# Optimization experiments

Hardware: AMD Instinct MI355X
Metric: run time of the kernel (lower is better)

The kernel has to match this reference:

```python
import jax, jax.numpy as jnp
import numpy as np

FRACTION = 0.33  # from attn_type='query_selector_0.33'


def setup_inputs() -> dict:
    key = jax.random.key(0)
    k1, k2, k3, k4 = jax.random.split(key, 4)
    B, L, DIM_VAL, DIM_ATTN = 8, 4096, 64, 64
    scale = 1.0 / np.sqrt(DIM_VAL).astype(np.float32)
    x = jax.random.normal(k1, (B, L, DIM_VAL), dtype=jnp.float32)
    Wq = jax.random.normal(k2, (DIM_VAL, DIM_ATTN), dtype=jnp.float32) * scale
    Wk = jax.random.normal(k3, (DIM_VAL, DIM_ATTN), dtype=jnp.float32) * scale
    Wv = jax.random.normal(k4, (DIM_VAL, DIM_VAL), dtype=jnp.float32) * scale
    return {"x": x, "Wq": Wq, "Wk": Wk, "Wv": Wv}


def reference(x, Wq, Wk, Wv):
    # Projections (bias-free Linears)
    Q = jnp.einsum('bld,de->ble', x, Wq)  # [B, L, Da]
    K = jnp.einsum('bld,de->ble', x, Wk)  # [B, L, Da]
    V = jnp.einsum('bld,de->ble', x, Wv)  # [B, L, Dv]

    B, L_Q, Da = Q.shape
    l_Q = int((1.0 - FRACTION) * L_Q)  # static: shapes known at trace time

    # keys.topk(l_Q, dim=1).values -> per-channel top-l_Q along seq; mean over them
    K_top = jax.lax.top_k(jnp.swapaxes(K, 1, 2), l_Q)[0]  # [B, Da, l_Q]
    K_reduce = K_top.mean(axis=-1)                         # [B, Da]

    # score each query against the reduced key; pick top-l_Q queries
    sqk = jnp.einsum('bd,bld->bl', K_reduce, Q)            # [B, L_Q]
    indices = jax.lax.top_k(sqk, l_Q)[1]                   # [B, l_Q] int32

    # gather sampled queries
    Q_sample = jnp.take_along_axis(Q, indices[:, :, None], axis=1)  # [B, l_Q, Da]

    # dense attention for the sampled queries only
    scores = jnp.einsum('bqd,bkd->bqk', Q_sample, K) / jnp.sqrt(jnp.asarray(Da, Q.dtype))
    attn = jax.nn.softmax(scores, axis=-1)                 # [B, l_Q, L]
    out_sel = jnp.einsum('bqk,bkv->bqv', attn, V)          # [B, l_Q, Dv]

    # mean-filled result, scatter attention outputs to selected rows
    mean_values = V.mean(axis=-2)                          # [B, Dv]
    result = jnp.broadcast_to(mean_values[:, None, :], (B, L_Q, V.shape[-1]))
    result = result.at[jnp.arange(B)[:, None], indices].set(out_sel)
    return result
```

## Files before the change

kernel.cpp:

```cpp
#include <hip/hip_runtime.h>
#include <hip/hip_bf16.h>
#include <math.h>

#define BATCH 8
#define SEQ   4096
#define DIM   64
#define LQ    2744
#define QPB   128
#define NQB   22
#define QPAD  2816
#define KS    4
#define L2E   1.4426950408889634f
#define QSC   0.1803368801111204f

typedef _Float16 half8 __attribute__((ext_vector_type(8)));
typedef short    bs8   __attribute__((ext_vector_type(8)));
typedef float    fx16  __attribute__((ext_vector_type(16)));
typedef unsigned short ushort_t;

union UH { uint4 u4; half8 h; };
union UB { unsigned u[4]; uint4 u4; bs8 s; };

__device__ __forceinline__ unsigned pack_bf16(float a, float b) {
    __hip_bfloat162 h = __float22bfloat162_rn(make_float2(a, b));
    union { __hip_bfloat162 h; unsigned u; } cv; cv.h = h; return cv.u;
}

__device__ __forceinline__ unsigned f2sort(float f) {
    unsigned u = __float_as_uint(f);
    return (u & 0x80000000u) ? ~u : (u | 0x80000000u);
}
__device__ __forceinline__ float sort2f(unsigned u) {
    return __uint_as_float((u & 0x80000000u) ? (u & 0x7FFFFFFFu) : ~u);
}

__device__ void radix_select_4096(const unsigned* u, int k, unsigned* hist,
                                  unsigned* scan, unsigned* res) {
    const int t = threadIdx.x;
    if (t == 0) { res[0] = 0u; res[1] = (unsigned)k; }
    for (int pass = 3; pass >= 0; --pass) {
        const int shift = pass * 8;
        hist[t] = 0u;
        __syncthreads();
        const unsigned pref  = res[0];
        const unsigned kk    = res[1];
        const unsigned hmask = (pass == 3) ? 0u : (0xFFFFFFFFu << (shift + 8));
        for (int i = t; i < 4096; i += 256) {
            unsigned ui = u[i];
            if ((ui & hmask) == pref) atomicAdd(&hist[(ui >> shift) & 255u], 1u);
        }
        __syncthreads();
        const unsigned h = hist[t];
        unsigned s = h;
        scan[t] = s;
        __syncthreads();
#pragma unroll
        for (int ofs = 1; ofs < 256; ofs <<= 1) {
            unsigned add = (t + ofs < 256) ? scan[t + ofs] : 0u;
            __syncthreads();
            s += add;
            scan[t] = s;
            __syncthreads();
        }
        if (s >= kk && (s - h) < kk) {
            res[0] = pref | ((unsigned)t << shift);
            res[1] = kk - (s - h);
        }
        __syncthreads();
    }
}

__global__ __launch_bounds__(256) void proj_kernel(
    const float* __restrict__ x,  const float* __restrict__ Wq,
    const float* __restrict__ Wk, const float* __restrict__ Wv,
    float* __restrict__ Q, float* __restrict__ Kt,
    _Float16* __restrict__ Qh, _Float16* __restrict__ Kh,
    ushort_t* __restrict__ Vt, float* __restrict__ meanacc) {
    const int rt = blockIdx.x, b = blockIdx.y, t = threadIdx.x;
    __shared__ float4 xs4[64 * 17];
    __shared__ float  red[4][64];
    {
        const float4* xg = (const float4*)(x + ((size_t)b * SEQ + rt * 64) * DIM);
        for (int i = 0; i < 4; ++i) {
            int s = t + 256 * i;
            xs4[(s >> 4) * 17 + (s & 15)] = xg[s];
        }
    }
    __syncthreads();
    const int ch = t & 63, rg = t >> 6;
    float accq[16], acck[16], accv[16];
#pragma unroll
    for (int i = 0; i < 16; ++i) { accq[i] = 0.f; acck[i] = 0.f; accv[i] = 0.f; }
    for (int dc = 0; dc < 4; ++dc) {
        float wq[16], wk[16], wv[16];
#pragma unroll
        for (int dd = 0; dd < 16; ++dd) {
            int d = dc * 16 + dd;
            wq[dd] = Wq[d * 64 + ch]; wk[dd] = Wk[d * 64 + ch]; wv[dd] = Wv[d * 64 + ch];
        }
        for (int r = 0; r < 16; ++r) {
            const int row = rg * 16 + r;
            const float4* xr = &xs4[row * 17 + dc * 4];
            float xv[16];
            float4 a0 = xr[0], a1 = xr[1], a2 = xr[2], a3 = xr[3];
            xv[0]=a0.x; xv[1]=a0.y; xv[2]=a0.z; xv[3]=a0.w;
            xv[4]=a1.x; xv[5]=a1.y; xv[6]=a1.z; xv[7]=a1.w;
            xv[8]=a2.x; xv[9]=a2.y; xv[10]=a2.z; xv[11]=a2.w;
            xv[12]=a3.x; xv[13]=a3.y; xv[14]=a3.z; xv[15]=a3.w;
#pragma unroll
            for (int dd = 0; dd < 16; ++dd) {
                accq[r] = fmaf(xv[dd], wq[dd], accq[r]);
                acck[r] = fmaf(xv[dd], wk[dd], acck[r]);
                accv[r] = fmaf(xv[dd], wv[dd], accv[r]);
            }
        }
    }
    const int rowbase = rt * 64 + rg * 16;
    float sv = 0.f;
#pragma unroll
    for (int r = 0; r < 16; ++r) {
        size_t o = ((size_t)b * SEQ + rowbase + r) * DIM + ch;
        Q[o]  = accq[r];
        Qh[o] = (_Float16)(accq[r] * QSC);
        Kh[o] = (_Float16)acck[r];
        sv += accv[r];
    }
    float4* ktp = (float4*)(Kt + ((size_t)b * 64 + ch) * SEQ + rowbase);
    ktp[0] = make_float4(acck[0], acck[1], acck[2], acck[3]);
    ktp[1] = make_float4(acck[4], acck[5], acck[6], acck[7]);
    ktp[2] = make_float4(acck[8], acck[9], acck[10], acck[11]);
    ktp[3] = make_float4(acck[12], acck[13], acck[14], acck[15]);
    {
        unsigned pk[8];
#pragma unroll
        for (int i = 0; i < 8; ++i) pk[i] = pack_bf16(accv[2*i], accv[2*i+1]);
        uint4* vp = (uint4*)(Vt + ((size_t)(b * 64 + ch)) * SEQ + rowbase);
        vp[0] = make_uint4(pk[0], pk[1], pk[4], pk[5]);
        vp[1] = make_uint4(pk[2], pk[3], pk[6], pk[7]);
    }
    red[rg][ch] = sv;
    __syncthreads();
    if (rg == 0)
        atomicAdd(&meanacc[b * 64 + ch],
                  red[0][ch] + red[1][ch] + red[2][ch] + red[3][ch]);
}

__global__ __launch_bounds__(256) void kmean_kernel(const float* __restrict__ Kt,
                                                    float* __restrict__ Kred) {
    __shared__ unsigned u[4096];
    __shared__ unsigned hist[256];
    __shared__ unsigned scan[256];
    __shared__ unsigned res[2];
    __shared__ float rsum[4];
    const int bc = blockIdx.x, t = threadIdx.x;
    const float4* c4 = (const float4*)(Kt + (size_t)bc * SEQ);
    for (int i = t; i < 1024; i += 256) {
        float4 v = c4[i];
        u[i*4+0] = f2sort(v.x); u[i*4+1] = f2sort(v.y);
        u[i*4+2] = f2sort(v.z); u[i*4+3] = f2sort(v.w);
    }
    __syncthreads();
    radix_select_4096(u, LQ, hist, scan, res);
    const unsigned Tu = res[0];
    const int krem = (int)res[1];
    float loc = 0.f;
    for (int i = t; i < 4096; i += 256)
        if (u[i] > Tu) loc += sort2f(u[i]);
    for (int msk = 1; msk < 64; msk <<= 1) loc += __shfl_xor(loc, msk, 64);
    if ((t & 63) == 0) rsum[t >> 6] = loc;
    __syncthreads();
    if (t == 0) {
        float s = rsum[0] + rsum[1] + rsum[2] + rsum[3] + (float)krem * sort2f(Tu);
        Kred[bc] = s / (float)LQ;
    }
}

__global__ __launch_bounds__(256) void sqk_kernel(const float* __restrict__ Q,
                                                  const float* __restrict__ Kred,
                                                  float* __restrict__ sqk) {
    const int b = blockIdx.y, l = blockIdx.x * 256 + threadIdx.x;
    __shared__ float kr[64];
    if (threadIdx.x < 64) kr[threadIdx.x] = Kred[b * 64 + threadIdx.x];
    __syncthreads();
    const float4* q = (const float4*)(Q + ((size_t)b * SEQ + l) * DIM);
    float s = 0.f;
#pragma unroll
    for (int i = 0; i < 16; ++i) {
        float4 v = q[i];
        s = fmaf(v.x, kr[i*4+0], s); s = fmaf(v.y, kr[i*4+1], s);
        s = fmaf(v.z, kr[i*4+2], s); s = fmaf(v.w, kr[i*4+3], s);
    }
    sqk[b * SEQ + l] = s;
}

__global__ __launch_bounds__(256) void select_kernel(const float* __restrict__ sqk,
                                                     int* __restrict__ sel) {
    __shared__ unsigned u[4096];
    __shared__ unsigned hist[256];
    __shared__ unsigned scan[256];
    __shared__ unsigned res[2];
    __shared__ int eq_idx[256];
    __shared__ int cnts[2];
    const int b = blockIdx.x, t = threadIdx.x;
    const float* col = sqk + (size_t)b * SEQ;
    for (int i = t; i < 4096; i += 256) u[i] = f2sort(col[i]);
    if (t < 2) cnts[t] = 0;
    __syncthreads();
    radix_select_4096(u, LQ, hist, scan, res);
    const unsigned Tu = res[0];
    const int krem = (int)res[1];
    int* selb = sel + b * QPAD;
    for (int i = t; i < 4096; i += 256) {
        unsigned ui = u[i];
        if (ui > Tu) {
            int p = atomicAdd(&cnts[0], 1);
            selb[p] = i;
        } else if (ui == Tu) {
            int p = atomicAdd(&cnts[1], 1);
            if (p < 256) eq_idx[p] = i;
        }
    }
    __syncthreads();
    if (t == 0) {
        int ng = cnts[0];
        int ne = cnts[1] < 256 ? cnts[1] : 256;
        for (int i = 1; i < ne; ++i) {
            int v = eq_idx[i], j = i - 1;
            while (j >= 0 && eq_idx[j] > v) { eq_idx[j+1] = eq_idx[j]; --j; }
            eq_idx[j+1] = v;
        }
        for (int j = 0; j < krem; ++j) selb[ng + j] = eq_idx[j];
        for (int j = LQ; j < QPAD; ++j) selb[j] = selb[LQ - 1];
    }
}

__global__ __launch_bounds__(256) void fill_kernel(const float* __restrict__ meanacc,
                                                   float* __restrict__ out) {
    const int idx = blockIdx.x * 256 + threadIdx.x;
    if (idx >= BATCH * SEQ * 16) return;
    const int b = idx >> 16, c = idx & 15;
    const float inv = 1.0f / (float)SEQ;
    float4 mv = make_float4(meanacc[b*64 + c*4 + 0] * inv,
                            meanacc[b*64 + c*4 + 1] * inv,
                            meanacc[b*64 + c*4 + 2] * inv,
                            meanacc[b*64 + c*4 + 3] * inv);
    ((float4*)out)[idx] = mv;
}

__global__ __launch_bounds__(256) void attn_kernel(
    const ushort_t* __restrict__ Qh, const ushort_t* __restrict__ Kh,
    const ushort_t* __restrict__ Vt, const int* __restrict__ sel,
    float* __restrict__ pl, float* __restrict__ pout) {
    const int qt = blockIdx.x, ks = blockIdx.y, b = blockIdx.z;
    const int t = threadIdx.x, w = t >> 6, lane = t & 63;
    const int col = lane & 31, h = lane >> 5;

    __shared__ ushort_t Ktile[2][32 * 64];
    __shared__ ushort_t Vtile[2][32 * 64];

    half8 qf[4];
    {
        const int q = qt * QPB + w * 32 + col;
        const int row = sel[b * QPAD + q];
        const uint4* qg = (const uint4*)(Qh + ((size_t)b * SEQ + row) * DIM);
#pragma unroll
        for (int m = 0; m < 4; ++m) { UH u; u.u4 = qg[2 * m + h]; qf[m] = u.h; }
    }

    fx16 O0, O1;
#pragma unroll
    for (int r = 0; r < 16; ++r) { O0[r] = 0.f; O1[r] = 0.f; }
    float l = 0.f;

    const int srow = t >> 3, sgr = t & 7;
    const int lg = sgr ^ (srow & 7);
    const int vD = lg >> 2, vc = (lg >> 1) & 1, vh = lg & 1;
    const size_t kgbase = ((size_t)b * SEQ + ks * 1024 + srow) * DIM + 8 * lg;
    const size_t vgbase = ((size_t)(b * DIM + srow + 32 * vD)) * SEQ
                          + ks * 1024 + vc * 16 + vh * 8;

    uint4 kreg = *(const uint4*)(Kh + kgbase);
    uint4 vreg = *(const uint4*)(Vt + vgbase);

    for (int tile = 0; tile < 32; ++tile) {
        const int buf = tile & 1;
        *(uint4*)&Ktile[buf][srow * 64 + sgr * 8] = kreg;
        *(uint4*)&Vtile[buf][srow * 64 + sgr * 8] = vreg;
        __syncthreads();
        if (tile < 31) {
            kreg = *(const uint4*)(Kh + kgbase + (size_t)(tile + 1) * 32 * DIM);
            vreg = *(const uint4*)(Vt + vgbase + (size_t)(tile + 1) * 32);
        }
        fx16 S;
#pragma unroll
        for (int r = 0; r < 16; ++r) S[r] = 0.f;
#pragma unroll
        for (int m = 0; m < 4; ++m) {
            UH kf;
            kf.u4 = *(const uint4*)&Ktile[buf][col * 64 + 8 * ((2 * m + h) ^ (col & 7))];
            S = __builtin_amdgcn_mfma_f32_32x32x16_f16(kf.h, qf[m], S, 0, 0, 0);
        }
        float p[16];
#pragma unroll
        for (int r = 0; r < 16; ++r) p[r] = exp2f(S[r]);
#pragma unroll
        for (int r = 0; r < 16; ++r) l += p[r];
        UB A0, A1;
#pragma unroll
        for (int v = 0; v < 4; ++v) {
            A0.u[v] = pack_bf16(p[2 * v],     p[2 * v + 1]);
            A1.u[v] = pack_bf16(p[8 + 2 * v], p[8 + 2 * v + 1]);
        }
#pragma unroll
        for (int D = 0; D < 2; ++D) {
            fx16& O = D ? O1 : O0;
#pragma unroll
            for (int c = 0; c < 2; ++c) {
                UB vf;
                vf.u4 = *(const uint4*)&Vtile[buf][col * 64 + 8 * ((4 * D + 2 * c + h) ^ (col & 7))];
                O = __builtin_amdgcn_mfma_f32_32x32x16_bf16(c ? A1.s : A0.s, vf.s, O, 0, 0, 0);
            }
        }
    }

    l += __shfl_xor(l, 32);

    const int qg0 = qt * QPB + w * 32;
    const size_t base = (size_t)b * QPAD + qg0;
#pragma unroll
    for (int D = 0; D < 2; ++D) {
        const fx16& O = D ? O1 : O0;
#pragma unroll
        for (int r = 0; r < 16; ++r) {
            const int q = (r & 3) + 8 * (r >> 2) + 4 * h;
            atomicAdd(&pout[(base + q) * DIM + D * 32 + col], O[r]);
        }
    }
    if (h == 0) atomicAdd(&pl[base + col], l);
}

__global__ __launch_bounds__(256) void comb_kernel(
    const float* __restrict__ pl, const float* __restrict__ pout,
    const int* __restrict__ sel, float* __restrict__ out) {
    const int idx = blockIdx.x * 256 + threadIdx.x;
    if (idx >= BATCH * LQ * 16) return;
    const int b = idx / (LQ * 16);
    const int r = idx % (LQ * 16);
    const int qs = r >> 4, c = r & 15;
    const size_t s0 = (size_t)b * QPAD + qs;
    const float inv = 1.0f / pl[s0];
    float4 a = ((const float4*)(pout + s0 * DIM))[c];
    float4 o = make_float4(a.x * inv, a.y * inv, a.z * inv, a.w * inv);
    const int row = sel[b * QPAD + qs];
    ((float4*)(out + ((size_t)b * SEQ + row) * DIM))[c] = o;
}

extern "C" void kernel_launch(void* const* d_in, const int* in_sizes, int n_in,
                              void* d_out, int out_size, void* d_ws, size_t ws_size,
                              hipStream_t stream) {
    const float* x  = (const float*)d_in[0];
    const float* Wq = (const float*)d_in[1];
    const float* Wk = (const float*)d_in[2];
    const float* Wv = (const float*)d_in[3];
    float* out = (float*)d_out;
    char* wsb  = (char*)d_ws;

    float*    Q       = (float*)(wsb);
    _Float16* Qh      = (_Float16*)(wsb + 8388608);
    _Float16* Kh      = (_Float16*)(wsb + 12582912);
    ushort_t* Vt      = (ushort_t*)(wsb + 16777216);
    float*    meanacc = (float*)(wsb + 20971520);
    float*    Kred    = (float*)(wsb + 20973568);
    float*    sqk     = (float*)(wsb + 20975616);
    int*      sel     = (int*)(wsb + 21106688);
    float*    Kt      = (float*)(wsb + 21196800);
    float*    pout    = (float*)(wsb + 21196800);
    float*    pl      = (float*)(wsb + 21196800 + 5767168);

    hipMemsetAsync(meanacc, 0, 512 * sizeof(float), stream);
    proj_kernel  <<<dim3(64, 8),          256, 0, stream>>>(x, Wq, Wk, Wv, Q, Kt,
                                                            Qh, Kh, Vt, meanacc);
    kmean_kernel <<<512,                  256, 0, stream>>>(Kt, Kred);
    sqk_kernel   <<<dim3(16, 8),          256, 0, stream>>>(Q, Kred, sqk);
    select_kernel<<<8,                    256, 0, stream>>>(sqk, sel);
    fill_kernel  <<<2048,                 256, 0, stream>>>(meanacc, out);
    hipMemsetAsync(pout, 0, 5767168 + 90112, stream);
    attn_kernel  <<<dim3(NQB, KS, BATCH), 256, 0, stream>>>((const ushort_t*)Qh,
                                                            (const ushort_t*)Kh,
                                                            Vt, sel, pl, pout);
    comb_kernel  <<<1372,                 256, 0, stream>>>(pl, pout, sel, out);
}
```

Measured before the change: 202.0 us.

## Fold mean fill into combine via inverse index map; drop fill kernel and memset

```diff
diff --git a/kernel.cpp b/kernel.cpp
--- a/kernel.cpp
+++ b/kernel.cpp
@@ -75,7 +75,7 @@
     const float* __restrict__ Wk, const float* __restrict__ Wv,
     float* __restrict__ Q, float* __restrict__ Kt,
     _Float16* __restrict__ Qh, _Float16* __restrict__ Kh,
-    ushort_t* __restrict__ Vt, float* __restrict__ meanacc) {
+    ushort_t* __restrict__ Vt, float* __restrict__ pmean) {
     const int rt = blockIdx.x, b = blockIdx.y, t = threadIdx.x;
     __shared__ float4 xs4[64 * 17];
     __shared__ float  red[4][64];
@@ -141,18 +141,25 @@
     red[rg][ch] = sv;
     __syncthreads();
     if (rg == 0)
-        atomicAdd(&meanacc[b * 64 + ch],
-                  red[0][ch] + red[1][ch] + red[2][ch] + red[3][ch]);
+        pmean[((size_t)b * 64 + ch) * 64 + rt] =
+            red[0][ch] + red[1][ch] + red[2][ch] + red[3][ch];
 }
 
 __global__ __launch_bounds__(256) void kmean_kernel(const float* __restrict__ Kt,
-                                                    float* __restrict__ Kred) {
+                                                    const float* __restrict__ pmean,
+                                                    float* __restrict__ Kred,
+                                                    float* __restrict__ meanfin) {
     __shared__ unsigned u[4096];
     __shared__ unsigned hist[256];
     __shared__ unsigned scan[256];
     __shared__ unsigned res[2];
     __shared__ float rsum[4];
     const int bc = blockIdx.x, t = threadIdx.x;
+    if (t < 64) {
+        float v = pmean[(size_t)bc * 64 + t];
+        for (int m = 1; m < 64; m <<= 1) v += __shfl_xor(v, m, 64);
+        if (t == 0) meanfin[bc] = v * (1.0f / (float)SEQ);
+    }
     const float4* c4 = (const float4*)(Kt + (size_t)bc * SEQ);
     for (int i = t; i < 1024; i += 256) {
         float4 v = c4[i];
@@ -194,7 +201,8 @@
 }
 
 __global__ __launch_bounds__(256) void select_kernel(const float* __restrict__ sqk,
-                                                     int* __restrict__ sel) {
+                                                     int* __restrict__ sel,
+                                                     int* __restrict__ inv) {
     __shared__ unsigned u[4096];
     __shared__ unsigned hist[256];
     __shared__ unsigned scan[256];
@@ -203,7 +211,11 @@
     __shared__ int cnts[2];
     const int b = blockIdx.x, t = threadIdx.x;
     const float* col = sqk + (size_t)b * SEQ;
-    for (int i = t; i < 4096; i += 256) u[i] = f2sort(col[i]);
+    int* invb = inv + (size_t)b * SEQ;
+    for (int i = t; i < 4096; i += 256) {
+        u[i] = f2sort(col[i]);
+        invb[i] = -1;
+    }
     if (t < 2) cnts[t] = 0;
     __syncthreads();
     radix_select_4096(u, LQ, hist, scan, res);
@@ -215,6 +227,7 @@
         if (ui > Tu) {
             int p = atomicAdd(&cnts[0], 1);
             selb[p] = i;
+            invb[i] = p;
         } else if (ui == Tu) {
             int p = atomicAdd(&cnts[1], 1);
             if (p < 256) eq_idx[p] = i;
@@ -229,25 +242,16 @@
             while (j >= 0 && eq_idx[j] > v) { eq_idx[j+1] = eq_idx[j]; --j; }
             eq_idx[j+1] = v;
         }
-        for (int j = 0; j < krem; ++j) selb[ng + j] = eq_idx[j];
-        for (int j = LQ; j < QPAD; ++j) selb[j] = selb[LQ - 1];
-    }
-}
-
-__global__ __launch_bounds__(256) void fill_kernel(const float* __restrict__ meanacc,
-                                                   float* __restrict__ out) {
-    const int idx = blockIdx.x * 256 + threadIdx.x;
-    if (idx >= BATCH * SEQ * 16) return;
-    const int b = idx >> 16, c = idx & 15;
-    const float inv = 1.0f / (float)SEQ;
-    float4 mv = make_float4(meanacc[b*64 + c*4 + 0] * inv,
-                            meanacc[b*64 + c*4 + 1] * inv,
-                            meanacc[b*64 + c*4 + 2] * inv,
-                            meanacc[b*64 + c*4 + 3] * inv);
-    ((float4*)out)[idx] = mv;
-}
-
-__global__ __launch_bounds__(256) void attn_kernel(
+        for (int j = 0; j < krem; ++j) {
+            selb[ng + j] = eq_idx[j];
+            invb[eq_idx[j]] = ng + j;
+        }
+    }
+    __syncthreads();
+    if (t < QPAD - LQ) selb[LQ + t] = selb[LQ - 1];
+}
+
+__global__ __launch_bounds__(256, 3) void attn_kernel(
     const ushort_t* __restrict__ Qh, const ushort_t* __restrict__ Kh,
     const ushort_t* __restrict__ Vt, const int* __restrict__ sel,
     float* __restrict__ pl, float* __restrict__ pout) {
@@ -266,6 +270,14 @@
 #pragma unroll
         for (int m = 0; m < 4; ++m) { UH u; u.u4 = qg[2 * m + h]; qf[m] = u.h; }
     }
+
+    int koff[4], voff[4];
+#pragma unroll
+    for (int m = 0; m < 4; ++m)
+        koff[m] = col * 64 + 8 * ((2 * m + h) ^ (col & 7));
+#pragma unroll
+    for (int i = 0; i < 4; ++i)
+        voff[i] = col * 64 + 8 * ((i * 2 + h) ^ (col & 7));
 
     fx16 O0, O1;
 #pragma unroll
@@ -297,7 +309,7 @@
 #pragma unroll
         for (int m = 0; m < 4; ++m) {
             UH kf;
-            kf.u4 = *(const uint4*)&Ktile[buf][col * 64 + 8 * ((2 * m + h) ^ (col & 7))];
+            kf.u4 = *(const uint4*)&Ktile[buf][koff[m]];
             S = __builtin_amdgcn_mfma_f32_32x32x16_f16(kf.h, qf[m], S, 0, 0, 0);
         }
         float p[16];
@@ -317,7 +329,7 @@
 #pragma unroll
             for (int c = 0; c < 2; ++c) {
                 UB vf;
-                vf.u4 = *(const uint4*)&Vtile[buf][col * 64 + 8 * ((4 * D + 2 * c + h) ^ (col & 7))];
+                vf.u4 = *(const uint4*)&Vtile[buf][voff[D * 2 + c]];
                 O = __builtin_amdgcn_mfma_f32_32x32x16_bf16(c ? A1.s : A0.s, vf.s, O, 0, 0, 0);
             }
         }
@@ -341,18 +353,24 @@
 
 __global__ __launch_bounds__(256) void comb_kernel(
     const float* __restrict__ pl, const float* __restrict__ pout,
-    const int* __restrict__ sel, float* __restrict__ out) {
+    const int* __restrict__ inv, const float* __restrict__ meanfin,
+    float* __restrict__ out) {
     const int idx = blockIdx.x * 256 + threadIdx.x;
-    if (idx >= BATCH * LQ * 16) return;
-    const int b = idx / (LQ * 16);
-    const int r = idx % (LQ * 16);
-    const int qs = r >> 4, c = r & 15;
-    const size_t s0 = (size_t)b * QPAD + qs;
-    const float inv = 1.0f / pl[s0];
-    float4 a = ((const float4*)(pout + s0 * DIM))[c];
-    float4 o = make_float4(a.x * inv, a.y * inv, a.z * inv, a.w * inv);
-    const int row = sel[b * QPAD + qs];
-    ((float4*)(out + ((size_t)b * SEQ + row) * DIM))[c] = o;
+    const int b = idx >> 16;
+    const int rc = idx & 65535;
+    const int row = rc >> 4, c = rc & 15;
+    const int p = inv[b * SEQ + row];
+    float4 o;
+    if (p >= 0) {
+        const size_t s0 = (size_t)b * QPAD + p;
+        const float invl = 1.0f / pl[s0];
+        float4 a = ((const float4*)(pout + s0 * DIM))[c];
+        o = make_float4(a.x * invl, a.y * invl, a.z * invl, a.w * invl);
+    } else {
+        o = make_float4(meanfin[b * 64 + c * 4 + 0], meanfin[b * 64 + c * 4 + 1],
+                        meanfin[b * 64 + c * 4 + 2], meanfin[b * 64 + c * 4 + 3]);
+    }
+    ((float4*)out)[idx] = o;
 }
 
 extern "C" void kernel_launch(void* const* d_in, const int* in_sizes, int n_in,
@@ -369,24 +387,24 @@
     _Float16* Qh      = (_Float16*)(wsb + 8388608);
     _Float16* Kh      = (_Float16*)(wsb + 12582912);
     ushort_t* Vt      = (ushort_t*)(wsb + 16777216);
-    float*    meanacc = (float*)(wsb + 20971520);
-    float*    Kred    = (float*)(wsb + 20973568);
-    float*    sqk     = (float*)(wsb + 20975616);
-    int*      sel     = (int*)(wsb + 21106688);
-    float*    Kt      = (float*)(wsb + 21196800);
-    float*    pout    = (float*)(wsb + 21196800);
-    float*    pl      = (float*)(wsb + 21196800 + 5767168);
-
-    hipMemsetAsync(meanacc, 0, 512 * sizeof(float), stream);
+    float*    pmean   = (float*)(wsb + 20971520);
+    float*    meanfin = (float*)(wsb + 21102592);
+    float*    Kred    = (float*)(wsb + 21104640);
+    float*    sqk     = (float*)(wsb + 21106688);
+    int*      sel     = (int*)(wsb + 21237760);
+    int*      inv     = (int*)(wsb + 21327872);
+    float*    Kt      = (float*)(wsb + 21458944);
+    float*    pout    = (float*)(wsb + 21458944);
+    float*    pl      = (float*)(wsb + 21458944 + 5767168);
+
     proj_kernel  <<<dim3(64, 8),          256, 0, stream>>>(x, Wq, Wk, Wv, Q, Kt,
-                                                            Qh, Kh, Vt, meanacc);
-    kmean_kernel <<<512,                  256, 0, stream>>>(Kt, Kred);
+                                                            Qh, Kh, Vt, pmean);
+    kmean_kernel <<<512,                  256, 0, stream>>>(Kt, pmean, Kred, meanfin);
     sqk_kernel   <<<dim3(16, 8),          256, 0, stream>>>(Q, Kred, sqk);
-    select_kernel<<<8,                    256, 0, stream>>>(sqk, sel);
-    fill_kernel  <<<2048,                 256, 0, stream>>>(meanacc, out);
+    select_kernel<<<8,                    256, 0, stream>>>(sqk, sel, inv);
     hipMemsetAsync(pout, 0, 5767168 + 90112, stream);
     attn_kernel  <<<dim3(NQB, KS, BATCH), 256, 0, stream>>>((const ushort_t*)Qh,
                                                             (const ushort_t*)Kh,
                                                             Vt, sel, pl, pout);
-    comb_kernel  <<<1372,                 256, 0, stream>>>(pl, pout, sel, out);
-}
+    comb_kernel  <<<2048,                 256, 0, stream>>>(pl, pout, inv, meanfin, out);
+}
```

New measurement: 195.0 us. 1.04x faster.
